# Performance work log

Hardware: AMD Instinct MI355X
Metric: run time of the kernel (lower is better)

The kernel has to match this reference:

```python
import jax, jax.numpy as jnp
import numpy as np

B, T, E, H = 4, 2048, 1024, 16
D = E // H  # head_dim = 64
THETA = 10000.0


def setup_inputs() -> dict:
    key = jax.random.key(0)
    ks = jax.random.split(key, 3)
    s = 0.02
    return {
        "x": jax.random.normal(ks[0], (B, T, E), jnp.float32),
        "W_attn": jax.random.normal(ks[1], (E, 3 * E), jnp.float32) * s,
        "b_attn": jnp.zeros((3 * E,), jnp.float32),
        "W_proj": jax.random.normal(ks[2], (E, E), jnp.float32) * s,
        "b_proj": jnp.zeros((E,), jnp.float32),
    }


def _rope(x, position_offset=0):
    # x: (B, H, T, D) -- interleaved even/odd pair rotation, as in apply_rope
    t, d = x.shape[2], x.shape[3]
    pos = jnp.arange(position_offset, position_offset + t, dtype=jnp.float32)
    inv_freq = 1.0 / (THETA ** (jnp.arange(0, d, 2, dtype=jnp.float32) / d))
    freqs = jnp.outer(pos, inv_freq)  # (T, D/2)
    cos = jnp.cos(freqs)[None, None].astype(x.dtype)
    sin = jnp.sin(freqs)[None, None].astype(x.dtype)
    xe = x[..., ::2]
    xo = x[..., 1::2]
    rot = jnp.stack((xe * cos - xo * sin, xe * sin + xo * cos), axis=-1)
    return rot.reshape(x.shape)


def reference(x, W_attn, b_attn, W_proj, b_proj):
    # fused qkv projection
    qkv = x @ W_attn + b_attn  # (B, T, 3E)
    q, k, v = jnp.split(qkv, 3, axis=-1)

    def heads(a):
        return a.reshape(B, T, H, D).transpose(0, 2, 1, 3)  # (B,H,T,D)

    q, k, v = heads(q), heads(k), heads(v)
    q = _rope(q)
    k = _rope(k)

    scores = jnp.einsum('bhqd,bhkd->bhqk', q, k) * (D ** -0.5)  # (B,H,T,T)
    causal = jnp.tril(jnp.ones((T, T), dtype=bool))
    scores = jnp.where(causal[None, None], scores, -jnp.inf)
    weights = jax.nn.softmax(scores, axis=-1)  # dropout p=0 (eval) -> identity

    out = jnp.einsum('bhqk,bhkd->bhqd', weights, v)
    out = out.transpose(0, 2, 1, 3).reshape(B, T, E)
    return out @ W_proj + b_proj
```

## Files before the change

### kernel.cpp

```cpp
#include <hip/hip_runtime.h>
#include <hip/hip_bf16.h>
#include <math.h>

#define TT 2048
#define HH 16

typedef short s16x8 __attribute__((ext_vector_type(8)));
typedef float f32x4 __attribute__((ext_vector_type(4)));

#define F4(p) (*reinterpret_cast<const float4*>(p))

__device__ __forceinline__ void gload16(const void* g, void* l) {
    __builtin_amdgcn_global_load_lds(
        (const __attribute__((address_space(1))) void*)g,
        (__attribute__((address_space(3))) void*)l, 16, 0, 0);
}

__device__ __forceinline__ ushort bf1(float a) {
    __hip_bfloat16 h = __float2bfloat16(a);
    union { __hip_bfloat16 h1; ushort u; } c; c.h1 = h; return c.u;
}
__device__ __forceinline__ uint pack_bf2(float a, float b) {
    __hip_bfloat162 h = __float22bfloat162_rn(make_float2(a, b));
    union { __hip_bfloat162 h2; uint u; } c; c.h2 = h; return c.u;
}

__device__ __forceinline__ float fexp2(float x) {
#if __has_builtin(__builtin_amdgcn_exp2f)
    return __builtin_amdgcn_exp2f(x);
#else
    float r; asm("v_exp_f32 %0, %1" : "=v"(r) : "v"(x)); return r;
#endif
}

__global__ __launch_bounds__(256) void prep_kernel(
    const float* __restrict__ x, const float* __restrict__ Wa,
    const float* __restrict__ Wp, ushort* __restrict__ xb,
    ushort* __restrict__ wat, ushort* __restrict__ wpt, float2* __restrict__ cs)
{
    __shared__ float tsh[64][65];
    const int blk = blockIdx.x;
    const int tid = threadIdx.x;

    if (blk < 256) {
        int idx = blk * 256 + tid;
        int t = idx >> 5;
        int i = idx & 31;
        double inv_d = exp(((double)(-2 * i) / 64.0) * log(10000.0));
        float invf = (float)inv_d;
        float freq = (float)t * invf;
        double df = (double)freq;
        cs[idx] = make_float2((float)cos(df), (float)sin(df));
    } else if (blk < 4352) {
        size_t i = (size_t)(blk - 256) * 2048 + (size_t)tid * 8;
        float4 a = F4(&x[i]); float4 b = F4(&x[i + 4]);
        s16x8 v;
        v[0] = bf1(a.x); v[1] = bf1(a.y); v[2] = bf1(a.z); v[3] = bf1(a.w);
        v[4] = bf1(b.x); v[5] = bf1(b.y); v[6] = bf1(b.z); v[7] = bf1(b.w);
        *reinterpret_cast<s16x8*>(&xb[i]) = v;
    } else {
        const float* in; ushort* out; int R, C, bx, by;
        if (blk < 5120) { int r = blk - 4352; in = Wa; out = wat; R = 1024; C = 3072; bx = r % 48; by = r / 48; }
        else            { int r = blk - 5120; in = Wp; out = wpt; R = 1024; C = 1024; bx = r & 15; by = r >> 4; }
        int r0 = by * 64, c0 = bx * 64;
        int ix = tid & 15, iy = tid >> 4;
#pragma unroll
        for (int j = 0; j < 4; ++j) {
            float4 v = F4(&in[(size_t)(r0 + iy + j * 16) * C + c0 + ix * 4]);
            tsh[iy + j * 16][ix * 4 + 0] = v.x;
            tsh[iy + j * 16][ix * 4 + 1] = v.y;
            tsh[iy + j * 16][ix * 4 + 2] = v.z;
            tsh[iy + j * 16][ix * 4 + 3] = v.w;
        }
        __syncthreads();
        int oc = tid >> 2, seg = tid & 3;
        s16x8 u0, u1;
#pragma unroll
        for (int i = 0; i < 8; ++i) u0[i] = bf1(tsh[seg * 16 + i][oc]);
#pragma unroll
        for (int i = 0; i < 8; ++i) u1[i] = bf1(tsh[seg * 16 + 8 + i][oc]);
        ushort* dst = &out[(size_t)(c0 + oc) * R + r0 + seg * 16];
        *reinterpret_cast<s16x8*>(dst) = u0;
        *reinterpret_cast<s16x8*>(dst + 8) = u1;
    }
}

__global__ __launch_bounds__(256, 2) void qkv_gemm_kernel(
    const ushort* __restrict__ xb,
    const ushort* __restrict__ wat,
    const float* __restrict__ bias,
    const float2* __restrict__ cs,
    ushort* __restrict__ qg, ushort* __restrict__ kg, ushort* __restrict__ vt)
{
    __shared__ ushort As[2][8192];
    __shared__ ushort Bs[2][8192];

    const int tid = threadIdx.x;
    const int lane = tid & 63, wid = tid >> 6;
    const int lane15 = lane & 15, kgrp = lane >> 4;
    const int wr = wid >> 1, wc = wid & 1;
    const int bid = blockIdx.x;
    const int sbid = (bid & 7) * 192 + (bid >> 3);
    const int n0 = (sbid % 24) * 128, m0 = (sbid / 24) * 128;
    const int swz = (lane15 & 7) << 4;
    const int srcsw = ((lane & 7) ^ ((lane >> 3) & 7)) * 8;
    const int kgrp16 = kgrp * 16;
    const float SCL = 0.125f * 1.44269504088896f;

    f32x4 acc[4][4] = {};

#define STAGE_QKV(bufi, kofs)                                                     \
    do {                                                                          \
        _Pragma("unroll")                                                         \
        for (int i_ = 0; i_ < 4; ++i_) {                                          \
            int c_ = wid * 4 + i_;                                                \
            gload16(xb + (size_t)(m0 + c_ * 8 + (lane >> 3)) * 1024 + (kofs) + srcsw, \
                    &As[bufi][c_ * 512]);                                         \
            gload16(wat + (size_t)(n0 + c_ * 8 + (lane >> 3)) * 1024 + (kofs) + srcsw, \
                    &Bs[bufi][c_ * 512]);                                         \
        }                                                                         \
    } while (0)

    STAGE_QKV(0, 0);
    int buf = 0;
    for (int kt = 0; kt < 16; ++kt) {
        __syncthreads();
        if (kt < 15) STAGE_QKV(buf ^ 1, (kt + 1) * 64);
        const char* Ap = (const char*)As[buf];
        const char* Bp = (const char*)Bs[buf];
#pragma unroll
        for (int ks = 0; ks < 2; ++ks) {
            s16x8 af[4], bfv[4];
            const int kb = (ks * 64 + kgrp16) ^ swz;
#pragma unroll
            for (int f = 0; f < 4; ++f) {
                int row = wr * 64 + f * 16 + lane15;
                af[f] = *reinterpret_cast<const s16x8*>(Ap + row * 128 + kb);
            }
#pragma unroll
            for (int g = 0; g < 4; ++g) {
                int row = wc * 64 + g * 16 + lane15;
                bfv[g] = *reinterpret_cast<const s16x8*>(Bp + row * 128 + kb);
            }
            __builtin_amdgcn_s_setprio(1);
#pragma unroll
            for (int f = 0; f < 4; ++f)
#pragma unroll
                for (int g = 0; g < 4; ++g)
                    acc[f][g] = __builtin_amdgcn_mfma_f32_16x16x32_bf16(
                        af[f], bfv[g], acc[f][g], 0, 0, 0);
            __builtin_amdgcn_s_setprio(0);
        }
        buf ^= 1;
    }

#pragma unroll
    for (int g = 0; g < 4; ++g) {
        const int n = n0 + wc * 64 + g * 16 + lane15;
        const int sec = n >> 10;
        const int e = n & 1023;
        const int hh = e >> 6, d = e & 63;
        const float bsv = bias[n];
#pragma unroll
        for (int f = 0; f < 4; ++f) {
            const int mb = m0 + wr * 64 + f * 16 + kgrp * 4;
            const int bb = mb >> 11;
            const int t0 = mb & 2047;
            if (sec == 2) {
                float v0 = acc[f][g][0] + bsv, v1 = acc[f][g][1] + bsv;
                float v2 = acc[f][g][2] + bsv, v3 = acc[f][g][3] + bsv;
                uint2 u = make_uint2(pack_bf2(v0, v1), pack_bf2(v2, v3));
                *reinterpret_cast<uint2*>(
                    &vt[((size_t)(bb * HH + hh) * 64 + d) * TT + t0]) = u;
            } else {
                ushort* dst = (sec == 0) ? qg : kg;
#pragma unroll
                for (int r = 0; r < 4; ++r) {
                    float v = acc[f][g][r] + bsv;
                    float p = __shfl_xor(v, 1);
                    float2 c2 = cs[(t0 + r) * 32 + (d >> 1)];
                    float rv = (d & 1) ? (p * c2.y + v * c2.x) : (v * c2.x - p * c2.y);
                    if (sec == 0) rv *= SCL;
                    dst[((size_t)(bb * HH + hh) * TT + t0 + r) * 64 + d] = bf1(rv);
                }
            }
        }
    }
#undef STAGE_QKV
}

__global__ __launch_bounds__(512, 6) void flash_kernel(
    const ushort* __restrict__ qg, const ushort* __restrict__ kg,
    const ushort* __restrict__ vt, ushort* __restrict__ aob)
{
    __shared__ ushort K_s[2][4096];
    __shared__ ushort V_s[2][4096];
    __shared__ ushort P_s[8192];

    const int tid = threadIdx.x;
    const int lane = tid & 63, wid = tid >> 6;
    const int lane15 = lane & 15, kgrp = lane >> 4;
    const int j = blockIdx.x;
    const int qt = 15 - (j >> 6);
    const int bh = j & 63;
    const int b = bh >> 4, h = bh & 15;
    const int q0 = qt * 128;
    const int wq = wid * 16;
    const int wq_abs = q0 + wq;
    const int swz = (lane15 & 7) << 4;
    const int srcsw = ((lane & 7) ^ ((lane >> 3) & 7)) * 8;
    const int kgrp16 = kgrp * 16;
    const int nt = 2 * qt + 2;

    const ushort* qp = qg + (size_t)bh * TT * 64;
    const ushort* kp = kg + (size_t)bh * TT * 64;
    const ushort* vp = vt + (size_t)bh * 64 * TT;
    char* Pw = (char*)P_s + wid * 2048;

#define STAGE_KV(bufi, kv0_)                                                      \
    do {                                                                          \
        gload16(kp + (size_t)((kv0_) + wid * 8 + (lane >> 3)) * 64 + srcsw,       \
                &K_s[bufi][wid * 512]);                                           \
        gload16(vp + (size_t)(wid * 8 + (lane >> 3)) * TT + (kv0_) + srcsw,       \
                &V_s[bufi][wid * 512]);                                           \
    } while (0)

    const ushort* qrow = qp + (size_t)(q0 + wq + lane15) * 64 + kgrp * 8;
    s16x8 qfr[2];
    qfr[0] = *reinterpret_cast<const s16x8*>(qrow);
    qfr[1] = *reinterpret_cast<const s16x8*>(qrow + 32);

    s16x8 ones;
#pragma unroll
    for (int e = 0; e < 8; ++e) ones[e] = (short)0x3F80;

    STAGE_KV(0, 0);

    f32x4 o[5] = {};
    float mreg = -3.0e38f;

    int buf = 0;
    for (int t = 0; t < nt; ++t) {
        __syncthreads();
        if (t + 1 < nt) STAGE_KV(buf ^ 1, (t + 1) * 64);

        const int kv0 = t * 64;
        if (kv0 <= wq_abs + 15) {
            const char* Kp = (const char*)K_s[buf];
            const char* Vp = (const char*)V_s[buf];

            f32x4 sacc[4] = {};
#pragma unroll
            for (int ks = 0; ks < 2; ++ks) {
                const int kb = (ks * 64 + kgrp16) ^ swz;
                s16x8 ka[4];
#pragma unroll
                for (int kf = 0; kf < 4; ++kf)
                    ka[kf] = *reinterpret_cast<const s16x8*>(Kp + (kf * 16 + lane15) * 128 + kb);
                __builtin_amdgcn_s_setprio(1);
#pragma unroll
                for (int kf = 0; kf < 4; ++kf)
                    sacc[kf] = __builtin_amdgcn_mfma_f32_16x16x32_bf16(
                        ka[kf], qfr[ks], sacc[kf], 0, 0, 0);
                __builtin_amdgcn_s_setprio(0);
            }

            const int qglob = q0 + wq + lane15;
            if (kv0 + 63 > wq_abs) {
#pragma unroll
                for (int kf = 0; kf < 4; ++kf)
#pragma unroll
                    for (int r = 0; r < 4; ++r) {
                        int kvg = kv0 + kf * 16 + kgrp * 4 + r;
                        if (kvg > qglob) sacc[kf][r] = -3.0e38f;
                    }
            }
            float t0m = fmaxf(fmaxf(sacc[0][0], sacc[0][1]), sacc[0][2]);
            float t1m = fmaxf(fmaxf(sacc[0][3], sacc[1][0]), sacc[1][1]);
            float t2m = fmaxf(fmaxf(sacc[1][2], sacc[1][3]), sacc[2][0]);
            float t3m = fmaxf(fmaxf(sacc[2][1], sacc[2][2]), sacc[2][3]);
            float t4m = fmaxf(fmaxf(sacc[3][0], sacc[3][1]), sacc[3][2]);
            float mx = fmaxf(fmaxf(fmaxf(t0m, t1m), fmaxf(t2m, t3m)),
                             fmaxf(t4m, sacc[3][3]));
            mx = fmaxf(mx, __shfl_xor(mx, 16));
            mx = fmaxf(mx, __shfl_xor(mx, 32));
            if (!__all(mx <= mreg + 8.f)) {
                const float mnew = fmaxf(mreg, mx);
                const float fs = fexp2(mreg - mnew);
#pragma unroll
                for (int df = 0; df < 5; ++df) o[df] *= fs;
                mreg = mnew;
            }
#pragma unroll
            for (int kf = 0; kf < 4; ++kf) {
                float p0 = fexp2(sacc[kf][0] - mreg);
                float p1 = fexp2(sacc[kf][1] - mreg);
                float p2 = fexp2(sacc[kf][2] - mreg);
                float p3 = fexp2(sacc[kf][3] - mreg);
                uint2 u = make_uint2(pack_bf2(p0, p1), pack_bf2(p2, p3));
                int kvb = (kf * 32 + kgrp * 8) ^ swz;
                *reinterpret_cast<uint2*>(Pw + lane15 * 128 + kvb) = u;
            }

#pragma unroll
            for (int ks = 0; ks < 2; ++ks) {
                const int kb = (ks * 64 + kgrp16) ^ swz;
                s16x8 va[4], pb;
#pragma unroll
                for (int df = 0; df < 4; ++df)
                    va[df] = *reinterpret_cast<const s16x8*>(Vp + (df * 16 + lane15) * 128 + kb);
                pb = *reinterpret_cast<const s16x8*>(Pw + lane15 * 128 + kb);
                __builtin_amdgcn_s_setprio(1);
#pragma unroll
                for (int df = 0; df < 4; ++df)
                    o[df] = __builtin_amdgcn_mfma_f32_16x16x32_bf16(
                        va[df], pb, o[df], 0, 0, 0);
                o[4] = __builtin_amdgcn_mfma_f32_16x16x32_bf16(
                    ones, pb, o[4], 0, 0, 0);
                __builtin_amdgcn_s_setprio(0);
            }
        }
        buf ^= 1;
    }

    {
        const float inv = 1.0f / o[4][0];
        const int row = wq + lane15;
#pragma unroll
        for (int df = 0; df < 4; ++df) {
            float p0 = o[df][0] * inv, p1 = o[df][1] * inv;
            float p2 = o[df][2] * inv, p3 = o[df][3] * inv;
            uint2 u = make_uint2(pack_bf2(p0, p1), pack_bf2(p2, p3));
            int db = (df * 32 + kgrp * 8) ^ ((row & 7) << 4);
            *reinterpret_cast<uint2*>((char*)P_s + row * 128 + db) = u;
        }
    }
    __syncthreads();
    {
        const int q = tid >> 2, seg = tid & 3;
        ushort* orow = aob + ((size_t)(b * TT + q0 + q)) * 1024 + h * 64 + seg * 16;
        int p0 = (seg * 32) ^ ((q & 7) << 4);
        int p1 = (seg * 32 + 16) ^ ((q & 7) << 4);
        s16x8 v0 = *reinterpret_cast<const s16x8*>((const char*)P_s + q * 128 + p0);
        s16x8 v1 = *reinterpret_cast<const s16x8*>((const char*)P_s + q * 128 + p1);
        *reinterpret_cast<s16x8*>(orow) = v0;
        *reinterpret_cast<s16x8*>(orow + 8) = v1;
    }
#undef STAGE_KV
}

__global__ __launch_bounds__(256, 2) void proj_gemm_kernel(
    const ushort* __restrict__ ab,
    const ushort* __restrict__ wpt,
    const float* __restrict__ bias,
    float* __restrict__ out)
{
    __shared__ ushort As[2][8192];
    __shared__ ushort Bs[2][8192];

    const int tid = threadIdx.x;
    const int lane = tid & 63, wid = tid >> 6;
    const int lane15 = lane & 15, kgrp = lane >> 4;
    const int wr = wid >> 1, wc = wid & 1;
    const int bid = blockIdx.x;
    const int sbid = (bid & 7) * 64 + (bid >> 3);
    const int n0 = (sbid & 7) * 128, m0 = (sbid >> 3) * 128;
    const int swz = (lane15 & 7) << 4;
    const int srcsw = ((lane & 7) ^ ((lane >> 3) & 7)) * 8;
    const int kgrp16 = kgrp * 16;

    f32x4 acc[4][4] = {};

#define STAGE_PRJ(bufi, kofs)                                                     \
    do {                                                                          \
        _Pragma("unroll")                                                         \
        for (int i_ = 0; i_ < 4; ++i_) {                                          \
            int c_ = wid * 4 + i_;                                                \
            gload16(ab + (size_t)(m0 + c_ * 8 + (lane >> 3)) * 1024 + (kofs) + srcsw, \
                    &As[bufi][c_ * 512]);                                         \
            gload16(wpt + (size_t)(n0 + c_ * 8 + (lane >> 3)) * 1024 + (kofs) + srcsw, \
                    &Bs[bufi][c_ * 512]);                                         \
        }                                                                         \
    } while (0)

    STAGE_PRJ(0, 0);
    int buf = 0;
    for (int kt = 0; kt < 16; ++kt) {
        __syncthreads();
        if (kt < 15) STAGE_PRJ(buf ^ 1, (kt + 1) * 64);
        const char* Ap = (const char*)As[buf];
        const char* Bp = (const char*)Bs[buf];
#pragma unroll
        for (int ks = 0; ks < 2; ++ks) {
            s16x8 af[4], bfv[4];
            const int kb = (ks * 64 + kgrp16) ^ swz;
#pragma unroll
            for (int f = 0; f < 4; ++f) {
                int row = wr * 64 + f * 16 + lane15;
                af[f] = *reinterpret_cast<const s16x8*>(Ap + row * 128 + kb);
            }
#pragma unroll
            for (int g = 0; g < 4; ++g) {
                int row = wc * 64 + g * 16 + lane15;
                bfv[g] = *reinterpret_cast<const s16x8*>(Bp + row * 128 + kb);
            }
            __builtin_amdgcn_s_setprio(1);
#pragma unroll
            for (int f = 0; f < 4; ++f)
#pragma unroll
                for (int g = 0; g < 4; ++g)
                    acc[f][g] = __builtin_amdgcn_mfma_f32_16x16x32_bf16(
                        af[f], bfv[g], acc[f][g], 0, 0, 0);
            __builtin_amdgcn_s_setprio(0);
        }
        buf ^= 1;
    }

#pragma unroll
    for (int g = 0; g < 4; ++g) {
        const int n = n0 + wc * 64 + g * 16 + lane15;
        const float bv = bias[n];
#pragma unroll
        for (int f = 0; f < 4; ++f)
#pragma unroll
            for (int r = 0; r < 4; ++r) {
                const int m = m0 + wr * 64 + f * 16 + kgrp * 4 + r;
                out[(size_t)m * 1024 + n] = acc[f][g][r] + bv;
            }
    }
#undef STAGE_PRJ
}

extern "C" void kernel_launch(void* const* d_in, const int* in_sizes, int n_in,
                              void* d_out, int out_size, void* d_ws, size_t ws_size,
                              hipStream_t stream) {
    const float* x  = (const float*)d_in[0];
    const float* Wa = (const float*)d_in[1];
    const float* ba = (const float*)d_in[2];
    const float* Wp = (const float*)d_in[3];
    const float* bp = (const float*)d_in[4];
    float* out = (float*)d_out;

    char* ws = (char*)d_ws;
    ushort* xb  = (ushort*)(ws + 0);
    ushort* wat = (ushort*)(ws + 16777216);
    ushort* wpt = (ushort*)(ws + 23068672);
    ushort* qg  = (ushort*)(ws + 25165824);
    ushort* kg  = (ushort*)(ws + 41943040);
    ushort* vtg = (ushort*)(ws + 58720256);
    ushort* aob = (ushort*)(ws + 75497472);
    float2* cs  = (float2*)(ws + 92274688);

    prep_kernel<<<dim3(5376), dim3(256), 0, stream>>>(x, Wa, Wp, xb, wat, wpt, cs);
    qkv_gemm_kernel<<<dim3(1536), dim3(256), 0, stream>>>(xb, wat, ba, cs, qg, kg, vtg);
    flash_kernel<<<dim3(1024), dim3(512), 0, stream>>>(qg, kg, vtg, aob);
    proj_gemm_kernel<<<dim3(512), dim3(256), 0, stream>>>(aob, wpt, bp, out);
}
```

Measured before the change: 258.0 us.

## Widen QKV GEMM tile to 128x256 with interleaved load/MFMA pipeline

```diff
diff --git a/kernel.cpp b/kernel.cpp
--- a/kernel.cpp
+++ b/kernel.cpp
@@ -9,6 +9,10 @@
 typedef float f32x4 __attribute__((ext_vector_type(4)));
 
 #define F4(p) (*reinterpret_cast<const float4*>(p))
+#define VMCNT(n) asm volatile("s_waitcnt vmcnt(" #n ")" ::: "memory")
+#define LGKM0 asm volatile("s_waitcnt lgkmcnt(0)" ::: "memory")
+#define SBAR __builtin_amdgcn_s_barrier()
+#define SCHEDB __builtin_amdgcn_sched_barrier(0)
 
 __device__ __forceinline__ void gload16(const void* g, void* l) {
     __builtin_amdgcn_global_load_lds(
@@ -24,7 +28,6 @@
     __hip_bfloat162 h = __float22bfloat162_rn(make_float2(a, b));
     union { __hip_bfloat162 h2; uint u; } c; c.h2 = h; return c.u;
 }
-
 __device__ __forceinline__ float fexp2(float x) {
 #if __has_builtin(__builtin_amdgcn_exp2f)
     return __builtin_amdgcn_exp2f(x);
@@ -49,8 +52,7 @@
         double inv_d = exp(((double)(-2 * i) / 64.0) * log(10000.0));
         float invf = (float)inv_d;
         float freq = (float)t * invf;
-        double df = (double)freq;
-        cs[idx] = make_float2((float)cos(df), (float)sin(df));
+        cs[idx] = make_float2((float)cos((double)freq), (float)sin((double)freq));
     } else if (blk < 4352) {
         size_t i = (size_t)(blk - 256) * 2048 + (size_t)tid * 8;
         float4 a = F4(&x[i]); float4 b = F4(&x[i + 4]);
@@ -92,78 +94,103 @@
     const float2* __restrict__ cs,
     ushort* __restrict__ qg, ushort* __restrict__ kg, ushort* __restrict__ vt)
 {
-    __shared__ ushort As[2][8192];
-    __shared__ ushort Bs[2][8192];
+    __shared__ ushort A_s[2][8192];
+    __shared__ ushort B_s[16384];
 
     const int tid = threadIdx.x;
     const int lane = tid & 63, wid = tid >> 6;
     const int lane15 = lane & 15, kgrp = lane >> 4;
-    const int wr = wid >> 1, wc = wid & 1;
+    const int wm = wid >> 1, wn = wid & 1;
     const int bid = blockIdx.x;
-    const int sbid = (bid & 7) * 192 + (bid >> 3);
-    const int n0 = (sbid % 24) * 128, m0 = (sbid / 24) * 128;
+    const int sbid = (bid & 7) * 96 + (bid >> 3);
+    const int n0 = (sbid % 12) * 256, m0 = (sbid / 12) * 128;
     const int swz = (lane15 & 7) << 4;
     const int srcsw = ((lane & 7) ^ ((lane >> 3) & 7)) * 8;
     const int kgrp16 = kgrp * 16;
     const float SCL = 0.125f * 1.44269504088896f;
 
-    f32x4 acc[4][4] = {};
-
-#define STAGE_QKV(bufi, kofs)                                                     \
+    f32x4 acc[4][8] = {};
+
+#define STG_A(pb, a, kofs)                                                        \
+    gload16(xb + (size_t)(m0 + (a) * 32 + wid * 8 + (lane >> 3)) * 1024 + (kofs) + srcsw, \
+            &A_s[pb][((a) * 32 + wid * 8) * 64])
+#define STG_B(bb, kofs)                                                           \
+    gload16(wat + (size_t)(n0 + (bb) * 32 + wid * 8 + (lane >> 3)) * 1024 + (kofs) + srcsw, \
+            &B_s[((bb) * 32 + wid * 8) * 64])
+#define RD_A(dst, q, ks)                                                          \
+    dst = *reinterpret_cast<const s16x8*>(Ap + (wm * 64 + (q) * 16 + lane15) * 128 + (((ks) * 64 + kgrp16) ^ swz))
+#define MFMA_Q(q, afr)                                                            \
     do {                                                                          \
+        __builtin_amdgcn_s_setprio(1);                                            \
         _Pragma("unroll")                                                         \
-        for (int i_ = 0; i_ < 4; ++i_) {                                          \
-            int c_ = wid * 4 + i_;                                                \
-            gload16(xb + (size_t)(m0 + c_ * 8 + (lane >> 3)) * 1024 + (kofs) + srcsw, \
-                    &As[bufi][c_ * 512]);                                         \
-            gload16(wat + (size_t)(n0 + c_ * 8 + (lane >> 3)) * 1024 + (kofs) + srcsw, \
-                    &Bs[bufi][c_ * 512]);                                         \
+        for (int g_ = 0; g_ < 8; ++g_) {                                          \
+            acc[q][g_] = __builtin_amdgcn_mfma_f32_16x16x32_bf16(afr[0], bf[g_][0], acc[q][g_], 0, 0, 0); \
+            acc[q][g_] = __builtin_amdgcn_mfma_f32_16x16x32_bf16(afr[1], bf[g_][1], acc[q][g_], 0, 0, 0); \
         }                                                                         \
+        __builtin_amdgcn_s_setprio(0);                                            \
     } while (0)
 
-    STAGE_QKV(0, 0);
-    int buf = 0;
+#pragma unroll
+    for (int a = 0; a < 4; ++a) STG_A(0, a, 0);
+#pragma unroll
+    for (int b = 0; b < 8; ++b) STG_B(b, 0);
+    VMCNT(0);
+    SBAR;
+
+    int abuf = 0;
     for (int kt = 0; kt < 16; ++kt) {
-        __syncthreads();
-        if (kt < 15) STAGE_QKV(buf ^ 1, (kt + 1) * 64);
-        const char* Ap = (const char*)As[buf];
-        const char* Bp = (const char*)Bs[buf];
-#pragma unroll
-        for (int ks = 0; ks < 2; ++ks) {
-            s16x8 af[4], bfv[4];
-            const int kb = (ks * 64 + kgrp16) ^ swz;
-#pragma unroll
-            for (int f = 0; f < 4; ++f) {
-                int row = wr * 64 + f * 16 + lane15;
-                af[f] = *reinterpret_cast<const s16x8*>(Ap + row * 128 + kb);
-            }
-#pragma unroll
-            for (int g = 0; g < 4; ++g) {
-                int row = wc * 64 + g * 16 + lane15;
-                bfv[g] = *reinterpret_cast<const s16x8*>(Bp + row * 128 + kb);
-            }
-            __builtin_amdgcn_s_setprio(1);
-#pragma unroll
-            for (int f = 0; f < 4; ++f)
-#pragma unroll
-                for (int g = 0; g < 4; ++g)
-                    acc[f][g] = __builtin_amdgcn_mfma_f32_16x16x32_bf16(
-                        af[f], bfv[g], acc[f][g], 0, 0, 0);
-            __builtin_amdgcn_s_setprio(0);
-        }
-        buf ^= 1;
-    }
-
-#pragma unroll
-    for (int g = 0; g < 4; ++g) {
-        const int n = n0 + wc * 64 + g * 16 + lane15;
+        const int kn = (kt < 15 ? kt + 1 : kt) * 64;
+        const int ab2 = abuf ^ 1;
+        const char* Ap = (const char*)A_s[abuf];
+        const char* Bp = (const char*)B_s;
+
+        VMCNT(2);
+
+        s16x8 bf[8][2], af[2];
+#pragma unroll
+        for (int g = 0; g < 8; ++g) {
+            const int rb = (wn * 128 + g * 16 + lane15) * 128;
+            bf[g][0] = *reinterpret_cast<const s16x8*>(Bp + rb + (kgrp16 ^ swz));
+            bf[g][1] = *reinterpret_cast<const s16x8*>(Bp + rb + ((64 + kgrp16) ^ swz));
+        }
+        RD_A(af[0], 0, 0); RD_A(af[1], 0, 1);
+        STG_A(ab2, 0, kn); STG_A(ab2, 2, kn);
+        SBAR; LGKM0; SCHEDB;
+        MFMA_Q(0, af);
+        SBAR;
+
+        RD_A(af[0], 1, 0); RD_A(af[1], 1, 1);
+        STG_B(0, kn); STG_B(1, kn); STG_B(2, kn); STG_B(3, kn);
+        SBAR; LGKM0; SCHEDB;
+        MFMA_Q(1, af);
+        SBAR;
+
+        VMCNT(6);
+        RD_A(af[0], 2, 0); RD_A(af[1], 2, 1);
+        STG_B(4, kn); STG_B(5, kn); STG_B(6, kn); STG_B(7, kn);
+        SBAR; LGKM0; SCHEDB;
+        MFMA_Q(2, af);
+        SBAR;
+
+        RD_A(af[0], 3, 0); RD_A(af[1], 3, 1);
+        STG_A(ab2, 1, kn); STG_A(ab2, 3, kn);
+        SBAR; LGKM0; SCHEDB;
+        MFMA_Q(3, af);
+        SBAR;
+
+        abuf = ab2;
+    }
+
+#pragma unroll
+    for (int g = 0; g < 8; ++g) {
+        const int n = n0 + wn * 128 + g * 16 + lane15;
         const int sec = n >> 10;
         const int e = n & 1023;
         const int hh = e >> 6, d = e & 63;
         const float bsv = bias[n];
 #pragma unroll
         for (int f = 0; f < 4; ++f) {
-            const int mb = m0 + wr * 64 + f * 16 + kgrp * 4;
+            const int mb = m0 + wm * 64 + f * 16 + kgrp * 4;
             const int bb = mb >> 11;
             const int t0 = mb & 2047;
             if (sec == 2) {
@@ -186,7 +213,10 @@
             }
         }
     }
-#undef STAGE_QKV
+#undef STG_A
+#undef STG_B
+#undef RD_A
+#undef MFMA_Q
 }
 
 __global__ __launch_bounds__(512, 6) void flash_kernel(
@@ -350,10 +380,8 @@
 }
 
 __global__ __launch_bounds__(256, 2) void proj_gemm_kernel(
-    const ushort* __restrict__ ab,
-    const ushort* __restrict__ wpt,
-    const float* __restrict__ bias,
-    float* __restrict__ out)
+    const ushort* __restrict__ ab, const ushort* __restrict__ wpt,
+    const float* __restrict__ bias, float* __restrict__ out)
 {
     __shared__ ushort As[2][8192];
     __shared__ ushort Bs[2][8192];
@@ -395,15 +423,11 @@
             s16x8 af[4], bfv[4];
             const int kb = (ks * 64 + kgrp16) ^ swz;
 #pragma unroll
-            for (int f = 0; f < 4; ++f) {
-                int row = wr * 64 + f * 16 + lane15;
-                af[f] = *reinterpret_cast<const s16x8*>(Ap + row * 128 + kb);
-            }
-#pragma unroll
-            for (int g = 0; g < 4; ++g) {
-                int row = wc * 64 + g * 16 + lane15;
-                bfv[g] = *reinterpret_cast<const s16x8*>(Bp + row * 128 + kb);
-            }
+            for (int f = 0; f < 4; ++f)
+                af[f] = *reinterpret_cast<const s16x8*>(Ap + (wr * 64 + f * 16 + lane15) * 128 + kb);
+#pragma unroll
+            for (int g = 0; g < 4; ++g)
+                bfv[g] = *reinterpret_cast<const s16x8*>(Bp + (wc * 64 + g * 16 + lane15) * 128 + kb);
             __builtin_amdgcn_s_setprio(1);
 #pragma unroll
             for (int f = 0; f < 4; ++f)
@@ -452,7 +476,7 @@
     float2* cs  = (float2*)(ws + 92274688);
 
     prep_kernel<<<dim3(5376), dim3(256), 0, stream>>>(x, Wa, Wp, xb, wat, wpt, cs);
-    qkv_gemm_kernel<<<dim3(1536), dim3(256), 0, stream>>>(xb, wat, ba, cs, qg, kg, vtg);
+    qkv_gemm_kernel<<<dim3(768), dim3(256), 0, stream>>>(xb, wat, ba, cs, qg, kg, vtg);
     flash_kernel<<<dim3(1024), dim3(512), 0, stream>>>(qg, kg, vtg, aob);
     proj_gemm_kernel<<<dim3(512), dim3(256), 0, stream>>>(aob, wpt, bp, out);
 }
```

Measured after the change: 263.4 us. 2.1% more time.
